# Kernel tuning notes

Measured on AMD Instinct MI355X. Metric: run time of the kernel, lower is better.

## Reference

```python
import jax, jax.numpy as jnp
import numpy as np

N = 100000   # nodes
E = 1000000  # edges (before self-loops)
IN = 128     # in_channel
HID = 32     # hidden_channels
H1 = 8       # in_head
OUT = 40     # out_channel
NEG_SLOPE = 0.2


def setup_inputs() -> dict:
    key = jax.random.key(0)
    ks = jax.random.split(key, 12)
    s = 0.05
    return {
        "x0": jax.random.normal(ks[0], (N, IN), jnp.float32),
        "W1": jax.random.normal(ks[1], (IN, H1 * HID), jnp.float32) * s,
        "att_src1": jax.random.normal(ks[2], (H1, HID), jnp.float32) * s,
        "att_dst1": jax.random.normal(ks[3], (H1, HID), jnp.float32) * s,
        "b1": jnp.zeros((H1 * HID,), jnp.float32),
        "W2": jax.random.normal(ks[4], (H1 * HID, 1 * HID), jnp.float32) * s,
        "att_src2": jax.random.normal(ks[5], (1, HID), jnp.float32) * s,
        "att_dst2": jax.random.normal(ks[6], (1, HID), jnp.float32) * s,
        "b2": jnp.zeros((HID,), jnp.float32),
        "linW": jax.random.normal(ks[7], (HID, OUT), jnp.float32) * s,
        "linb": jnp.zeros((OUT,), jnp.float32),
        "edge_index": jax.random.randint(ks[8], (2, E), 0, N, dtype=jnp.int64),
    }


def gat_conv(x, src, dst, W, att_src, att_dst, bias, concat):
    # PyG GATConv (eval mode): per-head linear, edge attention, dst-softmax, scatter-add
    H, C = att_src.shape
    h = (x @ W).reshape(N, H, C)                       # [N,H,C]
    a_src = jnp.sum(h * att_src[None], axis=-1)        # [N,H]
    a_dst = jnp.sum(h * att_dst[None], axis=-1)        # [N,H]
    alpha = jax.nn.leaky_relu(a_src[src] + a_dst[dst], NEG_SLOPE)  # [Etot,H]
    m = jax.ops.segment_max(alpha, dst, num_segments=N)           # [N,H]
    ea = jnp.exp(alpha - m[dst])
    denom = jax.ops.segment_sum(ea, dst, num_segments=N)
    w = ea / jnp.clip(denom, 1e-16, None)[dst]          # [Etot,H]
    out = jax.ops.segment_sum(w[:, :, None] * h[src], dst, num_segments=N)  # [N,H,C]
    out = out.reshape(N, H * C) if concat else jnp.mean(out, axis=1)
    return out + bias


def reference(x0, W1, att_src1, att_dst1, b1, W2, att_src2, att_dst2, b2, linW, linb, edge_index):
    # add self-loops (PyG add_self_loops=True default)
    loop = jnp.arange(N, dtype=edge_index.dtype)
    src = jnp.concatenate([edge_index[0], loop])
    dst = jnp.concatenate([edge_index[1], loop])
    # dropout layers are no-ops in eval mode
    x1 = gat_conv(x0, src, dst, W1, att_src1, att_dst1, b1, concat=True)   # [N, 8*HID]
    x2 = jax.nn.relu(x1)
    x2 = gat_conv(x2, src, dst, W2, att_src2, att_dst2, b2, concat=False)  # [N, HID]
    return x2 @ linW + linb                                                 # [N, OUT]
```

## Files before the change

### kernel.cpp

```cpp
#include <hip/hip_runtime.h>

#define N 100000
#define E 1000000
#define ETOT 1100000
#define NB1 391
#define NBE 4297
#define NPREP 2048
#define NBG 782
#define BUCKET 12500

typedef __attribute__((ext_vector_type(8))) short bf16x8;
typedef __attribute__((ext_vector_type(4))) float f32x4;
typedef __attribute__((ext_vector_type(2))) float f32x2;

__device__ __forceinline__ float lrelu(float x) { return x > 0.f ? x : 0.2f * x; }
__device__ __forceinline__ unsigned short f2b(float x) {
    unsigned u = __float_as_uint(x);
    return (unsigned short)((u + 0x7FFFu + ((u >> 16) & 1u)) >> 16);
}
__device__ __forceinline__ float b2f(unsigned short v) {
    return __uint_as_float(((unsigned)v) << 16);
}
__device__ __forceinline__ unsigned char f2q(float x) {
    return (unsigned char)(__builtin_amdgcn_cvt_pk_fp8_f32(x, x, 0, false) & 0xFF);
}

__global__ __launch_bounds__(256) void prep_kernel(const int* __restrict__ ei,
                                                   int* __restrict__ hist,
                                                   const float* __restrict__ W1,
                                                   const float* __restrict__ W2,
                                                   const float* __restrict__ att_src1,
                                                   const float* __restrict__ att_dst1,
                                                   unsigned short* __restrict__ W1T,
                                                   unsigned short* __restrict__ W2T) {
    const int b = blockIdx.x;
    const int t = threadIdx.x;
    if (b < NPREP) {
        const int k = b & 7;
        for (int w = b >> 3; w < NBE; w += 256) {
            const int e = w * 256 + t;
            if (e < ETOT) {
                int d = (e < E) ? ei[E + e] : (e - E);
                if (d / BUCKET == k) atomicAdd(&hist[d], 1);
            }
        }
        return;
    }
    const int bb = b - NPREP;
    if (bb < 128) {
        W1T[(size_t)t * 128 + bb] = f2b(W1[(size_t)bb * 256 + t]);
    } else if (bb < 160) {
        int n = bb - 128;
        W2T[(size_t)n * 256 + t] = f2b(W2[(size_t)t * 32 + n]);
    } else {
        int idx = (bb - 160) * 256 + t;
        int col = idx >> 7;
        int k = idx & 127;
        int h = col & 7;
        const float* att = (col < 8) ? att_src1 : att_dst1;
        float acc = 0.f;
#pragma unroll 8
        for (int j = 0; j < 32; j++) acc += W1[(size_t)k * 256 + h * 32 + j] * att[h * 32 + j];
        W1T[(size_t)(256 + col) * 128 + k] = f2b(acc);
    }
}

__global__ __launch_bounds__(256) void g1s_kernel(const float* __restrict__ x0,
                                                  const unsigned short* __restrict__ W1T,
                                                  unsigned char* __restrict__ h1,
                                                  float* __restrict__ a_src,
                                                  float* __restrict__ a_dst,
                                                  const int* __restrict__ hist,
                                                  int* __restrict__ rofs,
                                                  int* __restrict__ bsum) {
    __shared__ int sm[256];
    if (blockIdx.x >= NBG) {
        const int blk = blockIdx.x - NBG;
        const int t = threadIdx.x;
        const int i = blk * 256 + t;
        int v = (i < N) ? hist[i] : 0;
        sm[t] = v;
        __syncthreads();
#pragma unroll
        for (int off = 1; off < 256; off <<= 1) {
            int x = (t >= off) ? sm[t - off] : 0;
            __syncthreads();
            sm[t] += x;
            __syncthreads();
        }
        if (i < N) rofs[i] = sm[t] - v;
        if (t == 255) bsum[blk] = sm[255];
        return;
    }
    const int wv = threadIdx.x >> 6;
    const int lane = threadIdx.x & 63;
    const int quad = lane >> 4, c = lane & 15;
    const int base_m = blockIdx.x * 128 + wv * 32;
    const int l = c & 3;
    const unsigned sel1 = (l & 1) ? 0x07030501u : 0x02060004u;
    const unsigned sel2 = (l & 2) ? 0x07060302u : 0x01000504u;
    bf16x8 af[2][4];
#pragma unroll
    for (int mt = 0; mt < 2; mt++) {
        int row = base_m + mt * 16 + c;
        int rowc = row < N ? row : N - 1;
        const float* ap = x0 + (size_t)rowc * 128 + quad * 8;
#pragma unroll
        for (int ks = 0; ks < 4; ks++) {
            float4 lo = *(const float4*)(ap + ks * 32);
            float4 hi = *(const float4*)(ap + ks * 32 + 4);
            bf16x8 f;
            f[0] = (short)f2b(lo.x); f[1] = (short)f2b(lo.y);
            f[2] = (short)f2b(lo.z); f[3] = (short)f2b(lo.w);
            f[4] = (short)f2b(hi.x); f[5] = (short)f2b(hi.y);
            f[6] = (short)f2b(hi.z); f[7] = (short)f2b(hi.w);
            af[mt][ks] = f;
        }
    }
    for (int nt = 0; nt < 17; nt++) {
        f32x4 acc0 = {0.f, 0.f, 0.f, 0.f};
        f32x4 acc1 = {0.f, 0.f, 0.f, 0.f};
#pragma unroll
        for (int ks = 0; ks < 4; ks++) {
            bf16x8 bf = *(const bf16x8*)(W1T + (size_t)(nt * 16 + c) * 128 + ks * 32 + quad * 8);
            acc0 = __builtin_amdgcn_mfma_f32_16x16x32_bf16(af[0][ks], bf, acc0, 0, 0, 0);
            acc1 = __builtin_amdgcn_mfma_f32_16x16x32_bf16(af[1][ks], bf, acc1, 0, 0, 0);
        }
        if (nt < 16) {
            const int colb = nt * 16 + (c & 12);
            unsigned w0 = __builtin_amdgcn_cvt_pk_fp8_f32(acc0[0], acc0[1], 0u, false);
            w0 = __builtin_amdgcn_cvt_pk_fp8_f32(acc0[2], acc0[3], w0, true);
            unsigned w1 = __builtin_amdgcn_cvt_pk_fp8_f32(acc1[0], acc1[1], 0u, false);
            w1 = __builtin_amdgcn_cvt_pk_fp8_f32(acc1[2], acc1[3], w1, true);
            unsigned p0 = (unsigned)__shfl_xor((int)w0, 1, 64);
            unsigned p1 = (unsigned)__shfl_xor((int)w1, 1, 64);
            unsigned x0t = __builtin_amdgcn_perm(w0, p0, sel1);
            unsigned x1t = __builtin_amdgcn_perm(w1, p1, sel1);
            unsigned q0 = (unsigned)__shfl_xor((int)x0t, 2, 64);
            unsigned q1 = (unsigned)__shfl_xor((int)x1t, 2, 64);
            unsigned t0 = __builtin_amdgcn_perm(x0t, q0, sel2);
            unsigned t1 = __builtin_amdgcn_perm(x1t, q1, sel2);
            int r0 = base_m + quad * 4 + l;
            if (r0 < N) *(unsigned*)(h1 + (size_t)r0 * 256 + colb) = t0;
            int r1 = base_m + 16 + quad * 4 + l;
            if (r1 < N) *(unsigned*)(h1 + (size_t)r1 * 256 + colb) = t1;
        } else {
            float* dst = (c < 8) ? a_src : a_dst;
            int hh = c & 7;
#pragma unroll
            for (int r = 0; r < 4; r++) {
                int row0 = base_m + quad * 4 + r;
                if (row0 < N) dst[(size_t)row0 * 8 + hh] = acc0[r];
                int row1 = base_m + 16 + quad * 4 + r;
                if (row1 < N) dst[(size_t)row1 * 8 + hh] = acc1[r];
            }
        }
    }
}

__global__ __launch_bounds__(256) void scan23_kernel(int* __restrict__ rofs,
                                                     const int* __restrict__ bsum,
                                                     int* __restrict__ cursor) {
    __shared__ int red[4];
    const int blk = blockIdx.x;
    const int t = threadIdx.x;
    int v = 0;
    for (int j = t; j < blk; j += 256) v += bsum[j];
#pragma unroll
    for (int off = 1; off < 64; off <<= 1) v += __shfl_xor(v, off, 64);
    if ((t & 63) == 0) red[t >> 6] = v;
    __syncthreads();
    const int prefix = (red[0] + red[1]) + (red[2] + red[3]);
    const int i = blk * 256 + t;
    if (i < N) {
        int r = rofs[i] + prefix;
        rofs[i] = r;
        cursor[i] = r;
    }
    if (i == 0) rofs[N] = ETOT;
}

__global__ __launch_bounds__(256) void scatter_kernel(const int* __restrict__ ei,
                                                      int* __restrict__ cursor,
                                                      int* __restrict__ esrc) {
    const int k = blockIdx.x & 7;
    for (int w = blockIdx.x >> 3; w < NBE; w += 256) {
        const int e = w * 256 + threadIdx.x;
        if (e >= ETOT) continue;
        int s, d;
        if (e < E) { s = ei[e]; d = ei[E + e]; } else { s = d = e - E; }
        if (d / BUCKET != k) continue;
        int pos = atomicAdd(&cursor[d], 1);
        esrc[pos] = s;
    }
}

__global__ __launch_bounds__(1024, 8) void s1g2_kernel(const int* __restrict__ esrc,
                                                       const int* __restrict__ rofs,
                                                       const float* __restrict__ a_src,
                                                       const float* __restrict__ a_dst,
                                                       const unsigned char* __restrict__ h1,
                                                       const float* __restrict__ b1,
                                                       const unsigned short* __restrict__ W2T,
                                                       const float* __restrict__ att_src2,
                                                       const float* __restrict__ att_dst2,
                                                       unsigned short* __restrict__ h2,
                                                       float* __restrict__ a_src2,
                                                       float* __restrict__ a_dst2) {
    __shared__ unsigned short smx[16 * 264];
    const int wv = threadIdx.x >> 6;
    const int lane = threadIdx.x & 63;
    const int n = blockIdx.x * 16 + wv;
    const int e_pa = lane >> 3;
    const int h_pa = lane & 7;
    const int hB = lane >> 3;
    const int rs = __builtin_amdgcn_readfirstlane(rofs[n]);
    const int re = __builtin_amdgcn_readfirstlane(rofs[n + 1]);
    const float ad_pa = a_dst[(size_t)n * 8 + h_pa];
    float dsum = 0.f;
    float4 Aa = {0, 0, 0, 0}, Ab = {0, 0, 0, 0};
    for (int j0 = rs; j0 < re; j0 += 8) {
        int jm = j0 + e_pa;
        int jc = jm < re ? jm : re - 1;
        int s8 = esrc[jc];
        float av = a_src[(size_t)s8 * 8 + h_pa];
        float ex = __expf(lrelu(av + ad_pa));
        float w = (jm < re) ? ex : 0.f;
        dsum += w;
#pragma unroll
        for (int e = 0; e < 8; e++) {
            float wb = __shfl(w, e * 8 + hB, 64);
            int se = __builtin_amdgcn_readlane(s8, e * 8);
            unsigned hv = ((const unsigned*)(h1 + (size_t)se * 256))[lane];
            f32x2 lo = __builtin_amdgcn_cvt_pk_f32_fp8(hv, false);
            f32x2 hi = __builtin_amdgcn_cvt_pk_f32_fp8(hv, true);
            if (e & 1) {
                Ab.x += wb * lo[0]; Ab.y += wb * lo[1];
                Ab.z += wb * hi[0]; Ab.w += wb * hi[1];
            } else {
                Aa.x += wb * lo[0]; Aa.y += wb * lo[1];
                Aa.z += wb * hi[0]; Aa.w += wb * hi[1];
            }
        }
    }
    dsum += __shfl_xor(dsum, 8, 64);
    dsum += __shfl_xor(dsum, 16, 64);
    dsum += __shfl_xor(dsum, 32, 64);
    float den = __shfl(dsum, hB, 64);
    float4 acc = {Aa.x + Ab.x, Aa.y + Ab.y, Aa.z + Ab.z, Aa.w + Ab.w};
    const float inv = 1.0f / den;
    float4 bb = ((const float4*)b1)[lane];
    float vx = acc.x * inv + bb.x, vy = acc.y * inv + bb.y;
    float vz = acc.z * inv + bb.z, vw = acc.w * inv + bb.w;
    vx = vx > 0.f ? vx : 0.f; vy = vy > 0.f ? vy : 0.f;
    vz = vz > 0.f ? vz : 0.f; vw = vw > 0.f ? vw : 0.f;
    ushort4 o = {f2b(vx), f2b(vy), f2b(vz), f2b(vw)};
    *(ushort4*)(smx + wv * 264 + lane * 4) = o;
    __syncthreads();
    if (threadIdx.x < 64) {
        const int quad = lane >> 4, c = lane & 15;
        const int base_m = blockIdx.x * 16;
        f32x4 g[2] = {{0, 0, 0, 0}, {0, 0, 0, 0}};
#pragma unroll
        for (int ks = 0; ks < 8; ks++) {
            bf16x8 a = *(const bf16x8*)(smx + c * 264 + ks * 32 + quad * 8);
            bf16x8 b0 = *(const bf16x8*)(W2T + (size_t)c * 256 + ks * 32 + quad * 8);
            bf16x8 b1v = *(const bf16x8*)(W2T + (size_t)(16 + c) * 256 + ks * 32 + quad * 8);
            g[0] = __builtin_amdgcn_mfma_f32_16x16x32_bf16(a, b0, g[0], 0, 0, 0);
            g[1] = __builtin_amdgcn_mfma_f32_16x16x32_bf16(a, b1v, g[1], 0, 0, 0);
        }
        float as0 = att_src2[c], as1 = att_src2[16 + c];
        float ad0 = att_dst2[c], ad1 = att_dst2[16 + c];
#pragma unroll
        for (int r = 0; r < 4; r++) {
            int row = base_m + quad * 4 + r;
            float v0 = g[0][r], v1 = g[1][r];
            float ps = v0 * as0 + v1 * as1;
            float pd = v0 * ad0 + v1 * ad1;
#pragma unroll
            for (int off = 1; off < 16; off <<= 1) {
                ps += __shfl_xor(ps, off, 64);
                pd += __shfl_xor(pd, off, 64);
            }
            h2[(size_t)row * 32 + c] = f2b(v0);
            h2[(size_t)row * 32 + 16 + c] = f2b(v1);
            if (c == 0) { a_src2[row] = ps; a_dst2[row] = pd; }
        }
    }
}

__global__ __launch_bounds__(256) void seg2_kernel(const int* __restrict__ esrc,
                                                   const int* __restrict__ rofs,
                                                   const float* __restrict__ a_src2,
                                                   const float* __restrict__ a_dst2,
                                                   const unsigned short* __restrict__ h2,
                                                   const float* __restrict__ b2,
                                                   const float* __restrict__ linW,
                                                   const float* __restrict__ linb,
                                                   float* __restrict__ out) {
    __shared__ float lws[32 * 41];
    __shared__ float vbuf[8][33];
    const int t = threadIdx.x;
    for (int i = t; i < 1280; i += 256) {
        int ci = i / 40, o = i - ci * 40;
        lws[ci * 41 + o] = linW[i];
    }
    const int n8 = t >> 5;
    const int c = t & 31;
    const int myk = t & 7;
    const int n = blockIdx.x * 8 + n8;
    const int rs = rofs[n], re = rofs[n + 1];
    const float ad = a_dst2[n];
    float dsum = 0.f;
    float A[8] = {0, 0, 0, 0, 0, 0, 0, 0};
    for (int j0 = rs; j0 < re; j0 += 8) {
        int sidx[8];
#pragma unroll
        for (int k = 0; k < 8; k++) {
            int j = j0 + k;
            sidx[k] = esrc[j < re ? j : re - 1];
        }
        float av = a_src2[sidx[myk]];
        float myw = (j0 + myk < re) ? __expf(lrelu(av + ad)) : 0.f;
        dsum += myw;
        unsigned short hb[8];
#pragma unroll
        for (int k = 0; k < 8; k++) hb[k] = h2[(size_t)sidx[k] * 32 + c];
#pragma unroll
        for (int k = 0; k < 8; k++) {
            float w = __shfl(myw, (t & 32) + k, 64);
            A[k] += w * b2f(hb[k]);
        }
    }
    dsum += __shfl_xor(dsum, 1, 64);
    dsum += __shfl_xor(dsum, 2, 64);
    dsum += __shfl_xor(dsum, 4, 64);
    float acc = ((A[0] + A[1]) + (A[2] + A[3])) + ((A[4] + A[5]) + (A[6] + A[7]));
    vbuf[n8][c] = acc / dsum + b2[c];
    __syncthreads();
    for (int idx = t; idx < 320; idx += 256) {
        int nn = idx / 40, o = idx - nn * 40;
        float s = linb[o];
#pragma unroll
        for (int ci = 0; ci < 32; ci++) s += vbuf[nn][ci] * lws[ci * 41 + o];
        out[(size_t)blockIdx.x * 320 + idx] = s;
    }
}

extern "C" void kernel_launch(void* const* d_in, const int* in_sizes, int n_in,
                              void* d_out, int out_size, void* d_ws, size_t ws_size,
                              hipStream_t stream) {
    const float* x0       = (const float*)d_in[0];
    const float* W1       = (const float*)d_in[1];
    const float* att_src1 = (const float*)d_in[2];
    const float* att_dst1 = (const float*)d_in[3];
    const float* b1       = (const float*)d_in[4];
    const float* W2       = (const float*)d_in[5];
    const float* att_src2 = (const float*)d_in[6];
    const float* att_dst2 = (const float*)d_in[7];
    const float* b2       = (const float*)d_in[8];
    const float* linW     = (const float*)d_in[9];
    const float* linb     = (const float*)d_in[10];
    const int*   ei       = (const int*)d_in[11];
    float* out = (float*)d_out;
    float* ws  = (float*)d_ws;

    unsigned char* h1    = (unsigned char*)ws;
    float* a_src1        = ws + 19200000;
    float* a_dst1        = ws + 20000000;
    unsigned short* h2   = (unsigned short*)(ws + 20800000);
    float* a_src2        = ws + 22400000;
    float* a_dst2        = ws + 22500000;
    unsigned short* W1T  = (unsigned short*)(ws + 22600000);
    unsigned short* W2T  = (unsigned short*)(ws + 22620000);
    int*   hist          = (int*)(ws + 22630000);
    int*   rofs          = (int*)(ws + 22730000);
    int*   cursor        = (int*)(ws + 22840000);
    int*   bsum          = (int*)(ws + 22940000);
    int*   esrc          = (int*)(ws + 22941000);

    hipMemsetAsync(hist, 0, (size_t)N * 4, stream);

    prep_kernel<<<NPREP + 168, 256, 0, stream>>>(ei, hist, W1, W2, att_src1, att_dst1, W1T, W2T);
    g1s_kernel<<<NBG + NB1, 256, 0, stream>>>(x0, W1T, h1, a_src1, a_dst1, hist, rofs, bsum);
    scan23_kernel<<<NB1, 256, 0, stream>>>(rofs, bsum, cursor);
    scatter_kernel<<<NPREP, 256, 0, stream>>>(ei, cursor, esrc);
    s1g2_kernel<<<N / 16, 1024, 0, stream>>>(esrc, rofs, a_src1, a_dst1, h1, b1,
                                             W2T, att_src2, att_dst2, h2, a_src2, a_dst2);
    seg2_kernel<<<N / 8, 256, 0, stream>>>(esrc, rofs, a_src2, a_dst2, h2, b2, linW, linb, out);
}
```

Baseline: 358.9 us.

## Load-balance layer-1 aggregation across waves via chunk prefix-scan and LDS atomics

After: 620.6 us. 72.9% more time.

```diff
diff --git a/kernel.cpp b/kernel.cpp
--- a/kernel.cpp
+++ b/kernel.cpp
@@ -207,26 +207,59 @@
                                                        unsigned short* __restrict__ h2,
                                                        float* __restrict__ a_src2,
                                                        float* __restrict__ a_dst2) {
+    __shared__ float xacc[16][256];
+    __shared__ float denl[16][8];
+    __shared__ int rr[17];
+    __shared__ int rbase[17];
     __shared__ unsigned short smx[16 * 264];
-    const int wv = threadIdx.x >> 6;
-    const int lane = threadIdx.x & 63;
-    const int n = blockIdx.x * 16 + wv;
+    const int t = threadIdx.x;
+    const int wv = t >> 6;
+    const int lane = t & 63;
+    const int n0 = blockIdx.x * 16;
+    float* xf = (float*)xacc;
+    xf[t] = 0.f; xf[t + 1024] = 0.f; xf[t + 2048] = 0.f; xf[t + 3072] = 0.f;
+    if (t < 128) ((float*)denl)[t] = 0.f;
+    if (t < 17) rr[t] = rofs[n0 + t];
+    __syncthreads();
+    if (wv == 0) {
+        int cnt = 0;
+        if (lane < 16) cnt = ((rr[lane + 1] - rr[lane]) + 7) >> 3;
+        int incl = cnt;
+#pragma unroll
+        for (int off = 1; off < 16; off <<= 1) {
+            int v = __shfl_up(incl, off, 64);
+            if (lane >= off) incl += v;
+        }
+        if (lane < 16) rbase[lane] = incl - cnt;
+        if (lane == 15) rbase[16] = incl;
+    }
+    __syncthreads();
+    const int T = rbase[16];
     const int e_pa = lane >> 3;
     const int h_pa = lane & 7;
     const int hB = lane >> 3;
-    const int rs = __builtin_amdgcn_readfirstlane(rofs[n]);
-    const int re = __builtin_amdgcn_readfirstlane(rofs[n + 1]);
-    const float ad_pa = a_dst[(size_t)n * 8 + h_pa];
-    float dsum = 0.f;
-    float4 Aa = {0, 0, 0, 0}, Ab = {0, 0, 0, 0};
-    for (int j0 = rs; j0 < re; j0 += 8) {
+    for (int c = wv; c < T; c += 16) {
+        int node = 0;
+#pragma unroll
+        for (int step = 8; step >= 1; step >>= 1) {
+            int cand = node + step;
+            if (cand <= 15 && rbase[cand] <= c) node = cand;
+        }
+        const int re_n = rr[node + 1];
+        const int j0 = rr[node] + ((c - rbase[node]) << 3);
         int jm = j0 + e_pa;
-        int jc = jm < re ? jm : re - 1;
+        int jc = jm < re_n ? jm : re_n - 1;
         int s8 = esrc[jc];
         float av = a_src[(size_t)s8 * 8 + h_pa];
-        float ex = __expf(lrelu(av + ad_pa));
-        float w = (jm < re) ? ex : 0.f;
-        dsum += w;
+        float ad = a_dst[(size_t)(n0 + node) * 8 + h_pa];
+        float ex = __expf(lrelu(av + ad));
+        float w = (jm < re_n) ? ex : 0.f;
+        float dpart = w;
+        dpart += __shfl_xor(dpart, 8, 64);
+        dpart += __shfl_xor(dpart, 16, 64);
+        dpart += __shfl_xor(dpart, 32, 64);
+        if (lane < 8) atomicAdd(&denl[node][lane], dpart);
+        float4 Aa = {0, 0, 0, 0}, Ab = {0, 0, 0, 0};
 #pragma unroll
         for (int e = 0; e < 8; e++) {
             float wb = __shfl(w, e * 8 + hB, 64);
@@ -242,22 +275,26 @@
                 Aa.z += wb * hi[0]; Aa.w += wb * hi[1];
             }
         }
-    }
-    dsum += __shfl_xor(dsum, 8, 64);
-    dsum += __shfl_xor(dsum, 16, 64);
-    dsum += __shfl_xor(dsum, 32, 64);
-    float den = __shfl(dsum, hB, 64);
-    float4 acc = {Aa.x + Ab.x, Aa.y + Ab.y, Aa.z + Ab.z, Aa.w + Ab.w};
-    const float inv = 1.0f / den;
-    float4 bb = ((const float4*)b1)[lane];
-    float vx = acc.x * inv + bb.x, vy = acc.y * inv + bb.y;
-    float vz = acc.z * inv + bb.z, vw = acc.w * inv + bb.w;
-    vx = vx > 0.f ? vx : 0.f; vy = vy > 0.f ? vy : 0.f;
-    vz = vz > 0.f ? vz : 0.f; vw = vw > 0.f ? vw : 0.f;
-    ushort4 o = {f2b(vx), f2b(vy), f2b(vz), f2b(vw)};
-    *(ushort4*)(smx + wv * 264 + lane * 4) = o;
-    __syncthreads();
-    if (threadIdx.x < 64) {
+        atomicAdd(&xacc[node][lane * 4 + 0], Aa.x + Ab.x);
+        atomicAdd(&xacc[node][lane * 4 + 1], Aa.y + Ab.y);
+        atomicAdd(&xacc[node][lane * 4 + 2], Aa.z + Ab.z);
+        atomicAdd(&xacc[node][lane * 4 + 3], Aa.w + Ab.w);
+    }
+    __syncthreads();
+    {
+        float den = denl[wv][hB];
+        float4 acc = *(float4*)&xacc[wv][lane * 4];
+        const float inv = 1.0f / den;
+        float4 bb = ((const float4*)b1)[lane];
+        float vx = acc.x * inv + bb.x, vy = acc.y * inv + bb.y;
+        float vz = acc.z * inv + bb.z, vw = acc.w * inv + bb.w;
+        vx = vx > 0.f ? vx : 0.f; vy = vy > 0.f ? vy : 0.f;
+        vz = vz > 0.f ? vz : 0.f; vw = vw > 0.f ? vw : 0.f;
+        ushort4 o = {f2b(vx), f2b(vy), f2b(vz), f2b(vw)};
+        *(ushort4*)(smx + wv * 264 + lane * 4) = o;
+    }
+    __syncthreads();
+    if (t < 64) {
         const int quad = lane >> 4, c = lane & 15;
         const int base_m = blockIdx.x * 16;
         f32x4 g[2] = {{0, 0, 0, 0}, {0, 0, 0, 0}};
```
